# Kernel tuning notes

Hardware: AMD Instinct MI355X
Metric: run time of the kernel (lower is better)

Reference implementation:

```python
import jax, jax.numpy as jnp
import numpy as np

C = 256
CQK = C // 8  # 32

def setup_inputs() -> dict:
    key = jax.random.key(0)
    ks = jax.random.split(key, 8)
    N, L = 8, 4096
    x = jax.random.normal(ks[0], (N, C, L), dtype=jnp.float32)
    s = 1.0 / np.sqrt(C)
    Wq = jax.random.normal(ks[1], (CQK, C), dtype=jnp.float32) * s
    bq = jnp.zeros((CQK,), dtype=jnp.float32)
    Wk = jax.random.normal(ks[2], (CQK, C), dtype=jnp.float32) * s
    bk = jnp.zeros((CQK,), dtype=jnp.float32)
    Wv = jax.random.normal(ks[3], (C, C), dtype=jnp.float32) * s
    bv = jnp.zeros((C,), dtype=jnp.float32)
    gamma = jnp.ones((1,), dtype=jnp.float32) * 0.5  # nonzero so output depends on attention
    return {"x": x, "Wq": Wq, "bq": bq, "Wk": Wk, "bk": bk, "Wv": Wv, "bv": bv, "gamma": gamma}

def reference(x, Wq, bq, Wk, bk, Wv, bv, gamma):
    # conv1d with kernel_size=1 == pointwise linear over channel dim
    q = jnp.einsum('ncl,oc->nol', x, Wq) + bq[None, :, None]   # (N, C/8, L)
    k = jnp.einsum('ncl,oc->nol', x, Wk) + bk[None, :, None]   # (N, C/8, L)
    v = jnp.einsum('ncl,oc->nol', x, Wv) + bv[None, :, None]   # (N, C, L)
    # energy[n, i, j] = q[n, :, i] . k[n, :, j]
    energy = jnp.einsum('nci,ncj->nij', q, k)                  # (N, L, L)
    attention = jax.nn.softmax(energy, axis=-1)
    # out[n, c, i] = sum_j v[n, c, j] * attention[n, i, j]
    out = jnp.einsum('ncj,nij->nci', v, attention)             # (N, C, L)
    return gamma * out + x
```

## Files before the change

kernel.cpp:

```cpp
#include <hip/hip_runtime.h>
#include <hip/hip_bf16.h>

#define NB 8
#define CC 256
#define LL 4096
#define CQ 32

typedef __bf16 bf16x8 __attribute__((ext_vector_type(8)));
typedef float f32x4 __attribute__((ext_vector_type(4)));
typedef unsigned short u16x4 __attribute__((ext_vector_type(4)));

union B8u { bf16x8 b; u16x4 h[2]; };
union P4u { u16x4 u; __bf16 e[4]; };

#define WS_QT  ((size_t)0)
#define WS_KT  ((size_t)1048576)
#define WS_VV  ((size_t)2097152)
#define WS_WQ  ((size_t)18874368)
#define WS_BQ  ((size_t)18882560)
#define WS_WK  ((size_t)18882592)
#define WS_BK  ((size_t)18890784)
#define WS_WV  ((size_t)18890816)
#define WS_BV  ((size_t)18956352)

__device__ __forceinline__ bool tag_is_bf16(const void* gamma_raw) {
  return *(const unsigned short*)gamma_raw != 0;
}
__device__ __forceinline__ float cvt_load(const void* p, size_t i, bool b16) {
  return b16 ? (float)((const __bf16*)p)[i] : ((const float*)p)[i];
}

__global__ __launch_bounds__(256) void convert_wb_kernel(
    const void* __restrict__ Wq, const void* __restrict__ bq,
    const void* __restrict__ Wk, const void* __restrict__ bk,
    const void* __restrict__ Wv, const void* __restrict__ bv,
    const void* __restrict__ gm, __bf16* __restrict__ ws)
{
  const bool b16 = tag_is_bf16(gm);
  int t = blockIdx.x * 256 + threadIdx.x;
  for (int i = t; i < 82240; i += 32 * 256) {
    float v; size_t dof;
    if (i < 8192)       { v = cvt_load(Wq, i, b16);         dof = WS_WQ + i; }
    else if (i < 8224)  { v = cvt_load(bq, i - 8192, b16);  dof = WS_BQ + (i - 8192); }
    else if (i < 16416) { v = cvt_load(Wk, i - 8224, b16);  dof = WS_WK + (i - 8224); }
    else if (i < 16448) { v = cvt_load(bk, i - 16416, b16); dof = WS_BK + (i - 16416); }
    else if (i < 81984) { v = cvt_load(Wv, i - 16448, b16); dof = WS_WV + (i - 16448); }
    else                { v = cvt_load(bv, i - 81984, b16); dof = WS_BV + (i - 81984); }
    ws[dof] = (__bf16)v;
  }
}

__global__ __launch_bounds__(256, 2) void proj_kernel(
    const void* __restrict__ x_raw, const void* __restrict__ gm_raw,
    __bf16* __restrict__ ws)
{
  const bool b16 = tag_is_bf16(gm_raw);
  const int bid = blockIdx.x;
  const int n = bid & 7, l0 = (bid >> 3) * 64;
  const int tid = threadIdx.x;
  const int w = tid >> 6, lane = tid & 63, li = lane & 15, qd = lane >> 4;

  __shared__ __align__(16) __bf16 tmp[64][72];
  __shared__ __align__(16) __bf16 xlt[64][264];

  for (int cb = 0; cb < 4; ++cb) {
    __syncthreads();
    #pragma unroll
    for (int p = 0; p < 2; ++p) {
      int cc = (tid >> 3) + p * 32;
      int lc = (tid & 7) * 8;
      size_t off = (size_t)n * CC * LL + (size_t)(cb * 64 + cc) * LL + l0 + lc;
      bf16x8 val;
      if (b16) {
        val = *(const bf16x8*)((const __bf16*)x_raw + off);
      } else {
        const float* xf = (const float*)x_raw + off;
        f32x4 a = *(const f32x4*)xf;
        f32x4 b = *(const f32x4*)(xf + 4);
        #pragma unroll
        for (int s = 0; s < 4; ++s) { val[s] = (__bf16)a[s]; val[s + 4] = (__bf16)b[s]; }
      }
      *(bf16x8*)(&tmp[cc][lc]) = val;
    }
    __syncthreads();
    #pragma unroll
    for (int p = 0; p < 2; ++p) {
      int lx = (tid >> 3) + p * 32;
      int cw = (tid & 7) * 8;
      bf16x8 o;
      #pragma unroll
      for (int s = 0; s < 8; ++s) o[s] = tmp[cw + s][lx];
      *(bf16x8*)(&xlt[lx][cb * 64 + cw]) = o;
    }
  }
  __syncthreads();

  const __bf16* Wqk = (w < 2) ? (ws + WS_WQ) : (ws + WS_WK);
  const __bf16* Wv  = ws + WS_WV;
  const int obase = (w & 1) * 16;

  f32x4 vacc[4][4];
  f32x4 qkacc[4];
  #pragma unroll
  for (int a = 0; a < 4; ++a) {
    qkacc[a] = f32x4{0, 0, 0, 0};
    #pragma unroll
    for (int b = 0; b < 4; ++b) vacc[a][b] = f32x4{0, 0, 0, 0};
  }

  for (int k0 = 0; k0 < CC; k0 += 32) {
    bf16x8 xf[4];
    #pragma unroll
    for (int lt = 0; lt < 4; ++lt)
      xf[lt] = *(const bf16x8*)(&xlt[lt * 16 + li][k0 + qd * 8]);
    bf16x8 wa = *(const bf16x8*)(Wqk + (size_t)(obase + li) * CC + k0 + qd * 8);
    #pragma unroll
    for (int lt = 0; lt < 4; ++lt)
      qkacc[lt] = __builtin_amdgcn_mfma_f32_16x16x32_bf16(wa, xf[lt], qkacc[lt], 0, 0, 0);
    #pragma unroll
    for (int ct = 0; ct < 4; ++ct) {
      bf16x8 wb = *(const bf16x8*)(Wv + (size_t)(w * 64 + ct * 16 + li) * CC + k0 + qd * 8);
      #pragma unroll
      for (int lt = 0; lt < 4; ++lt)
        vacc[lt][ct] = __builtin_amdgcn_mfma_f32_16x16x32_bf16(xf[lt], wb, vacc[lt][ct], 0, 0, 0);
    }
  }

  {
    const __bf16* bqk = (w < 2) ? (ws + WS_BQ) : (ws + WS_BK);
    __bf16* dqk = ((w < 2) ? (ws + WS_QT) : (ws + WS_KT)) + (size_t)n * LL * CQ;
    float bf[4];
    #pragma unroll
    for (int rr = 0; rr < 4; ++rr) bf[rr] = (float)bqk[obase + qd * 4 + rr];
    #pragma unroll
    for (int lt = 0; lt < 4; ++lt) {
      P4u pk;
      #pragma unroll
      for (int rr = 0; rr < 4; ++rr) pk.e[rr] = (__bf16)(qkacc[lt][rr] + bf[rr]);
      *(u16x4*)(dqk + (size_t)(l0 + lt * 16 + li) * CQ + obase + qd * 4) = pk.u;
    }
  }
  {
    __bf16* dv = ws + WS_VV + (size_t)n * 128 * CC * 32;
    #pragma unroll
    for (int ct = 0; ct < 4; ++ct) {
      int c = w * 64 + ct * 16 + li;
      float bvf = (float)(ws + WS_BV)[c];
      #pragma unroll
      for (int lt = 0; lt < 4; ++lt) {
        int jl = lt * 16 + qd * 4;
        int jb = (l0 + jl) >> 5, jj = jl & 31;
        P4u pk;
        #pragma unroll
        for (int rr = 0; rr < 4; ++rr) pk.e[rr] = (__bf16)(vacc[lt][ct][rr] + bvf);
        *(u16x4*)(dv + ((size_t)jb * CC + c) * 32 + jj) = pk.u;
      }
    }
  }
}

__global__ __launch_bounds__(1024, 4) void attn_kernel(
    const __bf16* __restrict__ ws, const void* __restrict__ x_raw,
    const void* __restrict__ gamma_raw, void* __restrict__ out_raw)
{
  const int bid = blockIdx.x;
  const int n = bid & 7, iblk = (bid >> 3) * 128;
  const int tid = threadIdx.x, w = tid >> 6, lane = tid & 63;
  const int li = lane & 15, qd = lane >> 4;
  const int it = w & 7, jh = w >> 3;
  const int cg = w & 7, jg = w >> 3;

  const __bf16* qtn = ws + WS_QT + (size_t)n * LL * CQ;
  const __bf16* ktn = ws + WS_KT + (size_t)n * LL * CQ;
  const __bf16* v2n = ws + WS_VV + (size_t)n * 128 * CC * 32;

  __shared__ __align__(16) __bf16 plds[2][4][8][16][36];
  __shared__ __align__(16) float  lbuf[16][16];
  __shared__ __align__(16) __bf16 olds[256][72];
  float* scratch = (float*)&plds[0][0][0][0][0];

  bf16x8 qfrag = *(const bf16x8*)(qtn + (size_t)(iblk + it * 16 + li) * CQ + qd * 8);
  const f32x4 zero = {0.f, 0.f, 0.f, 0.f};

  f32x4 oacc[16];
  #pragma unroll
  for (int t = 0; t < 16; ++t) oacc[t] = zero;
  float lp = 0.f;

  bf16x8 kf[4];
  #pragma unroll
  for (int u = 0; u < 4; ++u)
    kf[u] = *(const bf16x8*)(ktn + (size_t)(jh * 64 + u * 16 + li) * CQ + qd * 8);

  for (int js = 0; js < LL; js += 128) {
    const int buf = (js >> 7) & 1;
    bf16x8 vf[4];
    #pragma unroll
    for (int s = 0; s < 2; ++s) {
      const int jb = (js >> 5) + jg * 2 + s;
      #pragma unroll
      for (int ct = 0; ct < 2; ++ct)
        vf[s * 2 + ct] = *(const bf16x8*)(v2n + ((size_t)jb * CC + cg * 32 + ct * 16 + li) * 32 + qd * 8);
    }
    #pragma unroll
    for (int u = 0; u < 4; ++u) {
      f32x4 s = __builtin_amdgcn_mfma_f32_16x16x32_bf16(kf[u], qfrag, zero, 0, 0, 0);
      P4u pk;
      #pragma unroll
      for (int r = 0; r < 4; ++r) {
        float e = __expf(s[r]); lp += e; pk.e[r] = (__bf16)e;
      }
      *(u16x4*)(&plds[buf][jh * 2 + (u >> 1)][it][li][(u & 1) * 16 + qd * 4]) = pk.u;
    }
    {
      const int jn = (js + 128 < LL) ? (js + 128) : 0;
      #pragma unroll
      for (int u = 0; u < 4; ++u)
        kf[u] = *(const bf16x8*)(ktn + (size_t)(jn + jh * 64 + u * 16 + li) * CQ + qd * 8);
    }
    __syncthreads();
    #pragma unroll
    for (int s = 0; s < 2; ++s) {
      #pragma unroll
      for (int tt = 0; tt < 8; ++tt) {
        B8u ap;
        ap.b = *(const bf16x8*)(&plds[buf][jg * 2 + s][tt][li][qd * 8]);
        oacc[tt * 2 + 0] = __builtin_amdgcn_mfma_f32_16x16x32_bf16(ap.b, vf[s * 2 + 0], oacc[tt * 2 + 0], 0, 0, 0);
        oacc[tt * 2 + 1] = __builtin_amdgcn_mfma_f32_16x16x32_bf16(ap.b, vf[s * 2 + 1], oacc[tt * 2 + 1], 0, 0, 0);
      }
    }
  }

  lp += __shfl_xor(lp, 16);
  lp += __shfl_xor(lp, 32);
  lbuf[it * 2 + jh][li] = lp;
  __syncthreads();

  #pragma unroll
  for (int r = 0; r < 2; ++r) {
    if (jg == 1 && (cg >> 2) == r) {
      float* d = scratch + (size_t)(cg & 3) * 4096;
      #pragma unroll
      for (int t = 0; t < 16; ++t)
        *(f32x4*)(d + t * 256 + lane * 4) = oacc[t];
    }
    __syncthreads();
    if (jg == 0 && (cg >> 2) == r) {
      const float* s = scratch + (size_t)(cg & 3) * 4096;
      #pragma unroll
      for (int t = 0; t < 16; ++t)
        oacc[t] += *(const f32x4*)(s + t * 256 + lane * 4);
    }
    __syncthreads();
  }

  const bool b16 = tag_is_bf16(gamma_raw);
  const float gma = b16 ? (float)(*(const __bf16*)gamma_raw)
                        : (*(const float*)gamma_raw);

  f32x4 gi[8];
  if (jg == 0) {
    #pragma unroll
    for (int pp = 0; pp < 8; ++pp) {
      f32x4 l0v = *(const f32x4*)(&lbuf[pp * 2 + 0][qd * 4]);
      f32x4 l1v = *(const f32x4*)(&lbuf[pp * 2 + 1][qd * 4]);
      #pragma unroll
      for (int rr = 0; rr < 4; ++rr) gi[pp][rr] = gma / (l0v[rr] + l1v[rr]);
    }
  }

  const int ec = tid >> 5, i2 = (tid & 31) * 2;
  #pragma unroll
  for (int h = 0; h < 2; ++h) {
    if (jg == 0) {
      #pragma unroll
      for (int pi = 0; pi < 4; ++pi) {
        const int pp = h * 4 + pi;
        #pragma unroll
        for (int ct = 0; ct < 2; ++ct) {
          P4u pk;
          #pragma unroll
          for (int rr = 0; rr < 4; ++rr)
            pk.e[rr] = (__bf16)(oacc[pp * 2 + ct][rr] * gi[pp][rr]);
          *(u16x4*)(&olds[cg * 32 + ct * 16 + li][pi * 16 + qd * 4]) = pk.u;
        }
      }
    }
    __syncthreads();
    const int ibase = iblk + h * 64;
    if (b16) {
      const __bf16* xn = (const __bf16*)x_raw + (size_t)n * CC * LL;
      __bf16* outn = (__bf16*)out_raw + (size_t)n * CC * LL;
      for (int c = ec; c < CC; c += 32) {
        unsigned int ov = *(const unsigned int*)(&olds[c][i2]);
        unsigned int xv = *(const unsigned int*)(xn + (size_t)c * LL + ibase + i2);
        const __bf16* op = (const __bf16*)&ov;
        const __bf16* xp = (const __bf16*)&xv;
        unsigned int res;
        __bf16* rp = (__bf16*)&res;
        rp[0] = (__bf16)((float)op[0] + (float)xp[0]);
        rp[1] = (__bf16)((float)op[1] + (float)xp[1]);
        *(unsigned int*)(outn + (size_t)c * LL + ibase + i2) = res;
      }
    } else {
      const float* xn = (const float*)x_raw + (size_t)n * CC * LL;
      float* outn = (float*)out_raw + (size_t)n * CC * LL;
      for (int c = ec; c < CC; c += 32) {
        unsigned int ov = *(const unsigned int*)(&olds[c][i2]);
        const __bf16* op = (const __bf16*)&ov;
        float2 xv = *(const float2*)(xn + (size_t)c * LL + ibase + i2);
        float2 res;
        res.x = (float)op[0] + xv.x;
        res.y = (float)op[1] + xv.y;
        *(float2*)(outn + (size_t)c * LL + ibase + i2) = res;
      }
    }
    __syncthreads();
  }
}

extern "C" void kernel_launch(void* const* d_in, const int* in_sizes, int n_in,
                              void* d_out, int out_size, void* d_ws, size_t ws_size,
                              hipStream_t stream) {
  (void)in_sizes; (void)n_in; (void)out_size; (void)ws_size;
  __bf16* ws = (__bf16*)d_ws;

  hipLaunchKernelGGL(convert_wb_kernel, dim3(32), dim3(256), 0, stream,
                     d_in[1], d_in[2], d_in[3], d_in[4], d_in[5], d_in[6],
                     d_in[7], ws);
  hipLaunchKernelGGL(proj_kernel, dim3(512), dim3(256), 0, stream,
                     d_in[0], d_in[7], ws);
  hipLaunchKernelGGL(attn_kernel, dim3(256), dim3(1024), 0, stream,
                     (const __bf16*)ws, d_in[0], d_in[7], d_out);
}
```

Measured before the change: 200.5 us.

## Switch attention kernel to 32x32x16 MFMA tiles with swizzled LDS and exp2

Rewrites the attention kernel's inner loop to use 32x32x16 bf16 MFMA instructions instead of 16x16x32, changing the wave-to-tile mapping, the P-tile LDS layout (now a flat 128x128 buffer with XOR swizzle), and the cross-wave reduction. Q is pre-scaled by log2(e) in the projection kernel so the softmax can use the raw exp2 instruction instead of __expf. The normalizer is computed once into a shared linv array. Launch bounds drop from 4 to 2 blocks per CU hint, trading occupancy for more registers and larger accumulator tiles.

```diff
diff --git a/kernel.cpp b/kernel.cpp
--- a/kernel.cpp
+++ b/kernel.cpp
@@ -8,9 +8,9 @@
 
 typedef __bf16 bf16x8 __attribute__((ext_vector_type(8)));
 typedef float f32x4 __attribute__((ext_vector_type(4)));
+typedef float f32x16 __attribute__((ext_vector_type(16)));
 typedef unsigned short u16x4 __attribute__((ext_vector_type(4)));
 
-union B8u { bf16x8 b; u16x4 h[2]; };
 union P4u { u16x4 u; __bf16 e[4]; };
 
 #define WS_QT  ((size_t)0)
@@ -128,6 +128,7 @@
 
   {
     const __bf16* bqk = (w < 2) ? (ws + WS_BQ) : (ws + WS_BK);
+    const float qscl = (w < 2) ? 1.4426950408889634f : 1.0f;
     __bf16* dqk = ((w < 2) ? (ws + WS_QT) : (ws + WS_KT)) + (size_t)n * LL * CQ;
     float bf[4];
     #pragma unroll
@@ -136,7 +137,7 @@
     for (int lt = 0; lt < 4; ++lt) {
       P4u pk;
       #pragma unroll
-      for (int rr = 0; rr < 4; ++rr) pk.e[rr] = (__bf16)(qkacc[lt][rr] + bf[rr]);
+      for (int rr = 0; rr < 4; ++rr) pk.e[rr] = (__bf16)((qkacc[lt][rr] + bf[rr]) * qscl);
       *(u16x4*)(dqk + (size_t)(l0 + lt * 16 + li) * CQ + obase + qd * 4) = pk.u;
     }
   }
@@ -159,97 +160,131 @@
   }
 }
 
-__global__ __launch_bounds__(1024, 4) void attn_kernel(
+__global__ __launch_bounds__(1024, 2) void attn_kernel(
     const __bf16* __restrict__ ws, const void* __restrict__ x_raw,
     const void* __restrict__ gamma_raw, void* __restrict__ out_raw)
 {
   const int bid = blockIdx.x;
   const int n = bid & 7, iblk = (bid >> 3) * 128;
   const int tid = threadIdx.x, w = tid >> 6, lane = tid & 63;
-  const int li = lane & 15, qd = lane >> 4;
-  const int it = w & 7, jh = w >> 3;
-  const int cg = w & 7, jg = w >> 3;
+  const int cl = lane & 31, hi = lane >> 5;
+  const int jt = w & 3, it2 = w >> 2;
+  const int ig = w & 1, cg = (w >> 1) & 3, jg = w >> 3;
 
   const __bf16* qtn = ws + WS_QT + (size_t)n * LL * CQ;
   const __bf16* ktn = ws + WS_KT + (size_t)n * LL * CQ;
   const __bf16* v2n = ws + WS_VV + (size_t)n * 128 * CC * 32;
 
-  __shared__ __align__(16) __bf16 plds[2][4][8][16][36];
-  __shared__ __align__(16) float  lbuf[16][16];
-  __shared__ __align__(16) __bf16 olds[256][72];
-  float* scratch = (float*)&plds[0][0][0][0][0];
-
-  bf16x8 qfrag = *(const bf16x8*)(qtn + (size_t)(iblk + it * 16 + li) * CQ + qd * 8);
-  const f32x4 zero = {0.f, 0.f, 0.f, 0.f};
-
-  f32x4 oacc[16];
-  #pragma unroll
-  for (int t = 0; t < 16; ++t) oacc[t] = zero;
+  __shared__ __align__(16) __bf16 plds[2][128][128];
+  __shared__ __align__(16) float  lbuf[4][128];
+  __shared__ __align__(16) float  linv[128];
+  __shared__ __align__(16) __bf16 olds[256][68];
+  float* scratch = (float*)&plds[0][0][0];
+  char* pbase = (char*)&plds[0][0][0];
+
+  const unsigned swzp = (unsigned)(cl & 15) << 4;
+
+  const unsigned pw_base = (unsigned)(it2 * 32 + cl) * 256;
+  unsigned wcol[4];
+  #pragma unroll
+  for (int g = 0; g < 4; ++g)
+    wcol[g] = (unsigned)((jt * 64 + 16 * g + 8 * hi) ^ (int)swzp);
+
+  const unsigned rrow0 = (unsigned)((ig * 2 + 0) * 32 + cl) * 256;
+  const unsigned rrow1 = (unsigned)((ig * 2 + 1) * 32 + cl) * 256;
+  unsigned rcol[4];
+  #pragma unroll
+  for (int ch = 0; ch < 4; ++ch)
+    rcol[ch] = (unsigned)((jg * 128 + ch * 32 + hi * 16) ^ (int)swzp);
+
+  const bf16x8 qf0 = *(const bf16x8*)(qtn + (size_t)(iblk + it2 * 32 + cl) * CQ + hi * 8);
+  const bf16x8 qf1 = *(const bf16x8*)(qtn + (size_t)(iblk + it2 * 32 + cl) * CQ + 16 + hi * 8);
+
+  const f32x16 z16 = {0.f,0.f,0.f,0.f, 0.f,0.f,0.f,0.f,
+                      0.f,0.f,0.f,0.f, 0.f,0.f,0.f,0.f};
+  f32x16 acc[2][2];
+  acc[0][0] = z16; acc[0][1] = z16; acc[1][0] = z16; acc[1][1] = z16;
   float lp = 0.f;
 
-  bf16x8 kf[4];
-  #pragma unroll
-  for (int u = 0; u < 4; ++u)
-    kf[u] = *(const bf16x8*)(ktn + (size_t)(jh * 64 + u * 16 + li) * CQ + qd * 8);
+  bf16x8 kf0 = *(const bf16x8*)(ktn + (size_t)(jt * 32 + cl) * CQ + hi * 8);
+  bf16x8 kf1 = *(const bf16x8*)(ktn + (size_t)(jt * 32 + cl) * CQ + 16 + hi * 8);
 
   for (int js = 0; js < LL; js += 128) {
-    const int buf = (js >> 7) & 1;
-    bf16x8 vf[4];
-    #pragma unroll
-    for (int s = 0; s < 2; ++s) {
-      const int jb = (js >> 5) + jg * 2 + s;
+    char* pbyte = pbase + (((js >> 7) & 1) << 15);
+    bf16x8 vf[4][2];
+    #pragma unroll
+    for (int ch = 0; ch < 4; ++ch) {
+      const int jb = (js >> 5) + jg * 2 + (ch >> 1);
+      const int jlo = (ch & 1) * 16 + hi * 8;
       #pragma unroll
       for (int ct = 0; ct < 2; ++ct)
-        vf[s * 2 + ct] = *(const bf16x8*)(v2n + ((size_t)jb * CC + cg * 32 + ct * 16 + li) * 32 + qd * 8);
-    }
-    #pragma unroll
-    for (int u = 0; u < 4; ++u) {
-      f32x4 s = __builtin_amdgcn_mfma_f32_16x16x32_bf16(kf[u], qfrag, zero, 0, 0, 0);
+        vf[ch][ct] = *(const bf16x8*)(v2n + ((size_t)jb * CC + cg * 64 + ct * 32 + cl) * 32 + jlo);
+    }
+    const int jn = (js + 128 < LL) ? (js + 128) : 0;
+    const bf16x8 kn0 = *(const bf16x8*)(ktn + (size_t)(jn + jt * 32 + cl) * CQ + hi * 8);
+    const bf16x8 kn1 = *(const bf16x8*)(ktn + (size_t)(jn + jt * 32 + cl) * CQ + 16 + hi * 8);
+
+    f32x16 sv = __builtin_amdgcn_mfma_f32_32x32x16_bf16(kf0, qf0, z16, 0, 0, 0);
+    sv = __builtin_amdgcn_mfma_f32_32x32x16_bf16(kf1, qf1, sv, 0, 0, 0);
+    #pragma unroll
+    for (int g = 0; g < 4; ++g) {
+      float e0 = __builtin_amdgcn_exp2f(sv[g * 4 + 0]);
+      float e1 = __builtin_amdgcn_exp2f(sv[g * 4 + 1]);
+      float e2 = __builtin_amdgcn_exp2f(sv[g * 4 + 2]);
+      float e3 = __builtin_amdgcn_exp2f(sv[g * 4 + 3]);
+      lp += (e0 + e1) + (e2 + e3);
       P4u pk;
-      #pragma unroll
-      for (int r = 0; r < 4; ++r) {
-        float e = __expf(s[r]); lp += e; pk.e[r] = (__bf16)e;
-      }
-      *(u16x4*)(&plds[buf][jh * 2 + (u >> 1)][it][li][(u & 1) * 16 + qd * 4]) = pk.u;
-    }
-    {
-      const int jn = (js + 128 < LL) ? (js + 128) : 0;
-      #pragma unroll
-      for (int u = 0; u < 4; ++u)
-        kf[u] = *(const bf16x8*)(ktn + (size_t)(jn + jh * 64 + u * 16 + li) * CQ + qd * 8);
-    }
-    __syncthreads();
-    #pragma unroll
-    for (int s = 0; s < 2; ++s) {
-      #pragma unroll
-      for (int tt = 0; tt < 8; ++tt) {
-        B8u ap;
-        ap.b = *(const bf16x8*)(&plds[buf][jg * 2 + s][tt][li][qd * 8]);
-        oacc[tt * 2 + 0] = __builtin_amdgcn_mfma_f32_16x16x32_bf16(ap.b, vf[s * 2 + 0], oacc[tt * 2 + 0], 0, 0, 0);
-        oacc[tt * 2 + 1] = __builtin_amdgcn_mfma_f32_16x16x32_bf16(ap.b, vf[s * 2 + 1], oacc[tt * 2 + 1], 0, 0, 0);
-      }
-    }
-  }
-
-  lp += __shfl_xor(lp, 16);
+      pk.e[0] = (__bf16)e0; pk.e[1] = (__bf16)e1;
+      pk.e[2] = (__bf16)e2; pk.e[3] = (__bf16)e3;
+      *(u16x4*)(pbyte + pw_base + wcol[g]) = pk.u;
+    }
+    kf0 = kn0; kf1 = kn1;
+    __syncthreads();
+    #pragma unroll
+    for (int ch = 0; ch < 4; ++ch) {
+      const bf16x8 ap0 = *(const bf16x8*)(pbyte + rrow0 + rcol[ch]);
+      const bf16x8 ap1 = *(const bf16x8*)(pbyte + rrow1 + rcol[ch]);
+      acc[0][0] = __builtin_amdgcn_mfma_f32_32x32x16_bf16(ap0, vf[ch][0], acc[0][0], 0, 0, 0);
+      acc[0][1] = __builtin_amdgcn_mfma_f32_32x32x16_bf16(ap0, vf[ch][1], acc[0][1], 0, 0, 0);
+      acc[1][0] = __builtin_amdgcn_mfma_f32_32x32x16_bf16(ap1, vf[ch][0], acc[1][0], 0, 0, 0);
+      acc[1][1] = __builtin_amdgcn_mfma_f32_32x32x16_bf16(ap1, vf[ch][1], acc[1][1], 0, 0, 0);
+    }
+  }
+
   lp += __shfl_xor(lp, 32);
-  lbuf[it * 2 + jh][li] = lp;
+  if (hi == 0) lbuf[jt][it2 * 32 + cl] = lp;
   __syncthreads();
 
   #pragma unroll
   for (int r = 0; r < 2; ++r) {
-    if (jg == 1 && (cg >> 2) == r) {
-      float* d = scratch + (size_t)(cg & 3) * 4096;
-      #pragma unroll
-      for (int t = 0; t < 16; ++t)
-        *(f32x4*)(d + t * 256 + lane * 4) = oacc[t];
-    }
-    __syncthreads();
-    if (jg == 0 && (cg >> 2) == r) {
-      const float* s = scratch + (size_t)(cg & 3) * 4096;
-      #pragma unroll
-      for (int t = 0; t < 16; ++t)
-        oacc[t] += *(const f32x4*)(s + t * 256 + lane * 4);
+    if (jg == 1 && (cg & 1) == r) {
+      float* d = scratch + (size_t)(ig * 2 + (cg >> 1)) * 4096 + lane * 4;
+      #pragma unroll
+      for (int tl = 0; tl < 2; ++tl)
+        #pragma unroll
+        for (int ct = 0; ct < 2; ++ct)
+          #pragma unroll
+          for (int q = 0; q < 4; ++q) {
+            f32x4 v4 = { acc[tl][ct][q * 4 + 0], acc[tl][ct][q * 4 + 1],
+                         acc[tl][ct][q * 4 + 2], acc[tl][ct][q * 4 + 3] };
+            *(f32x4*)(d + (tl * 8 + ct * 4 + q) * 256) = v4;
+          }
+    }
+    __syncthreads();
+    if (jg == 0 && (cg & 1) == r) {
+      const float* s0 = scratch + (size_t)(ig * 2 + (cg >> 1)) * 4096 + lane * 4;
+      #pragma unroll
+      for (int tl = 0; tl < 2; ++tl)
+        #pragma unroll
+        for (int ct = 0; ct < 2; ++ct)
+          #pragma unroll
+          for (int q = 0; q < 4; ++q) {
+            const f32x4 v4 = *(const f32x4*)(s0 + (tl * 8 + ct * 4 + q) * 256);
+            acc[tl][ct][q * 4 + 0] += v4[0];
+            acc[tl][ct][q * 4 + 1] += v4[1];
+            acc[tl][ct][q * 4 + 2] += v4[2];
+            acc[tl][ct][q * 4 + 3] += v4[3];
+          }
     }
     __syncthreads();
   }
@@ -257,32 +292,29 @@
   const bool b16 = tag_is_bf16(gamma_raw);
   const float gma = b16 ? (float)(*(const __bf16*)gamma_raw)
                         : (*(const float*)gamma_raw);
-
-  f32x4 gi[8];
-  if (jg == 0) {
-    #pragma unroll
-    for (int pp = 0; pp < 8; ++pp) {
-      f32x4 l0v = *(const f32x4*)(&lbuf[pp * 2 + 0][qd * 4]);
-      f32x4 l1v = *(const f32x4*)(&lbuf[pp * 2 + 1][qd * 4]);
-      #pragma unroll
-      for (int rr = 0; rr < 4; ++rr) gi[pp][rr] = gma / (l0v[rr] + l1v[rr]);
-    }
-  }
+  if (tid < 128)
+    linv[tid] = gma / (lbuf[0][tid] + lbuf[1][tid] + lbuf[2][tid] + lbuf[3][tid]);
+  __syncthreads();
 
   const int ec = tid >> 5, i2 = (tid & 31) * 2;
   #pragma unroll
   for (int h = 0; h < 2; ++h) {
-    if (jg == 0) {
-      #pragma unroll
-      for (int pi = 0; pi < 4; ++pi) {
-        const int pp = h * 4 + pi;
+    if (jg == 0 && ig == h) {
+      #pragma unroll
+      for (int tl = 0; tl < 2; ++tl) {
         #pragma unroll
         for (int ct = 0; ct < 2; ++ct) {
-          P4u pk;
+          const int c = cg * 64 + ct * 32 + cl;
           #pragma unroll
-          for (int rr = 0; rr < 4; ++rr)
-            pk.e[rr] = (__bf16)(oacc[pp * 2 + ct][rr] * gi[pp][rr]);
-          *(u16x4*)(&olds[cg * 32 + ct * 16 + li][pi * 16 + qd * 4]) = pk.u;
+          for (int g = 0; g < 4; ++g) {
+            const int io = tl * 32 + 8 * g + 4 * hi;
+            const f32x4 gv = *(const f32x4*)&linv[h * 64 + io];
+            P4u pk;
+            #pragma unroll
+            for (int rr = 0; rr < 4; ++rr)
+              pk.e[rr] = (__bf16)(acc[tl][ct][g * 4 + rr] * gv[rr]);
+            *(u16x4*)(&olds[c][io]) = pk.u;
+          }
         }
       }
     }
```

New measurement: 370.4 us. 1.85x slower.

## Halve attention block size and drop split-j cross-wave accumulator reduction

Applied to the files above, without the earlier changes.

Each attention block now covers 64 query rows with 512 threads instead of 128 rows with 1024 threads, and the grid doubles to 512 blocks. Each wave now owns a 32-channel slice across the full 128-key step, so the split-key partial accumulators and their shared-memory reduction with extra barriers go away. V fragments are reloaded mid-step for the second key half, with a sched_barrier between the halves. This cuts accumulator registers and epilogue synchronisation and gives more blocks for load balance. In exchange, each block does twice the V loads per query row and K is re-read by twice as many blocks.

```diff
diff --git a/kernel.cpp b/kernel.cpp
--- a/kernel.cpp
+++ b/kernel.cpp
@@ -159,32 +159,31 @@
   }
 }
 
-__global__ __launch_bounds__(1024, 4) void attn_kernel(
+__global__ __launch_bounds__(512, 4) void attn_kernel(
     const __bf16* __restrict__ ws, const void* __restrict__ x_raw,
     const void* __restrict__ gamma_raw, void* __restrict__ out_raw)
 {
   const int bid = blockIdx.x;
-  const int n = bid & 7, iblk = (bid >> 3) * 128;
+  const int n = bid & 7, iblk = (bid >> 3) * 64;
   const int tid = threadIdx.x, w = tid >> 6, lane = tid & 63;
   const int li = lane & 15, qd = lane >> 4;
-  const int it = w & 7, jh = w >> 3;
-  const int cg = w & 7, jg = w >> 3;
+  const int it = w & 3, jh = w >> 2;
+  const int cg = w;
 
   const __bf16* qtn = ws + WS_QT + (size_t)n * LL * CQ;
   const __bf16* ktn = ws + WS_KT + (size_t)n * LL * CQ;
   const __bf16* v2n = ws + WS_VV + (size_t)n * 128 * CC * 32;
 
-  __shared__ __align__(16) __bf16 plds[2][4][8][16][36];
-  __shared__ __align__(16) float  lbuf[16][16];
+  __shared__ __align__(16) __bf16 plds[2][4][4][16][36];
+  __shared__ __align__(16) float  lbuf[8][16];
   __shared__ __align__(16) __bf16 olds[256][72];
-  float* scratch = (float*)&plds[0][0][0][0][0];
 
   bf16x8 qfrag = *(const bf16x8*)(qtn + (size_t)(iblk + it * 16 + li) * CQ + qd * 8);
   const f32x4 zero = {0.f, 0.f, 0.f, 0.f};
 
-  f32x4 oacc[16];
-  #pragma unroll
-  for (int t = 0; t < 16; ++t) oacc[t] = zero;
+  f32x4 oacc[8];
+  #pragma unroll
+  for (int t = 0; t < 8; ++t) oacc[t] = zero;
   float lp = 0.f;
 
   bf16x8 kf[4];
@@ -197,7 +196,7 @@
     bf16x8 vf[4];
     #pragma unroll
     for (int s = 0; s < 2; ++s) {
-      const int jb = (js >> 5) + jg * 2 + s;
+      const int jb = (js >> 5) + s;
       #pragma unroll
       for (int ct = 0; ct < 2; ++ct)
         vf[s * 2 + ct] = *(const bf16x8*)(v2n + ((size_t)jb * CC + cg * 32 + ct * 16 + li) * 32 + qd * 8);
@@ -222,9 +221,27 @@
     #pragma unroll
     for (int s = 0; s < 2; ++s) {
       #pragma unroll
-      for (int tt = 0; tt < 8; ++tt) {
+      for (int tt = 0; tt < 4; ++tt) {
         B8u ap;
-        ap.b = *(const bf16x8*)(&plds[buf][jg * 2 + s][tt][li][qd * 8]);
+        ap.b = *(const bf16x8*)(&plds[buf][s][tt][li][qd * 8]);
+        oacc[tt * 2 + 0] = __builtin_amdgcn_mfma_f32_16x16x32_bf16(ap.b, vf[s * 2 + 0], oacc[tt * 2 + 0], 0, 0, 0);
+        oacc[tt * 2 + 1] = __builtin_amdgcn_mfma_f32_16x16x32_bf16(ap.b, vf[s * 2 + 1], oacc[tt * 2 + 1], 0, 0, 0);
+      }
+    }
+    __builtin_amdgcn_sched_barrier(0);
+    #pragma unroll
+    for (int s = 0; s < 2; ++s) {
+      const int jb = (js >> 5) + 2 + s;
+      #pragma unroll
+      for (int ct = 0; ct < 2; ++ct)
+        vf[s * 2 + ct] = *(const bf16x8*)(v2n + ((size_t)jb * CC + cg * 32 + ct * 16 + li) * 32 + qd * 8);
+    }
+    #pragma unroll
+    for (int s = 0; s < 2; ++s) {
+      #pragma unroll
+      for (int tt = 0; tt < 4; ++tt) {
+        B8u ap;
+        ap.b = *(const bf16x8*)(&plds[buf][2 + s][tt][li][qd * 8]);
         oacc[tt * 2 + 0] = __builtin_amdgcn_mfma_f32_16x16x32_bf16(ap.b, vf[s * 2 + 0], oacc[tt * 2 + 0], 0, 0, 0);
         oacc[tt * 2 + 1] = __builtin_amdgcn_mfma_f32_16x16x32_bf16(ap.b, vf[s * 2 + 1], oacc[tt * 2 + 1], 0, 0, 0);
       }
@@ -236,86 +253,60 @@
   lbuf[it * 2 + jh][li] = lp;
   __syncthreads();
 
-  #pragma unroll
-  for (int r = 0; r < 2; ++r) {
-    if (jg == 1 && (cg >> 2) == r) {
-      float* d = scratch + (size_t)(cg & 3) * 4096;
-      #pragma unroll
-      for (int t = 0; t < 16; ++t)
-        *(f32x4*)(d + t * 256 + lane * 4) = oacc[t];
-    }
-    __syncthreads();
-    if (jg == 0 && (cg >> 2) == r) {
-      const float* s = scratch + (size_t)(cg & 3) * 4096;
-      #pragma unroll
-      for (int t = 0; t < 16; ++t)
-        oacc[t] += *(const f32x4*)(s + t * 256 + lane * 4);
-    }
-    __syncthreads();
-  }
-
   const bool b16 = tag_is_bf16(gamma_raw);
   const float gma = b16 ? (float)(*(const __bf16*)gamma_raw)
                         : (*(const float*)gamma_raw);
 
-  f32x4 gi[8];
-  if (jg == 0) {
-    #pragma unroll
-    for (int pp = 0; pp < 8; ++pp) {
-      f32x4 l0v = *(const f32x4*)(&lbuf[pp * 2 + 0][qd * 4]);
-      f32x4 l1v = *(const f32x4*)(&lbuf[pp * 2 + 1][qd * 4]);
-      #pragma unroll
-      for (int rr = 0; rr < 4; ++rr) gi[pp][rr] = gma / (l0v[rr] + l1v[rr]);
-    }
-  }
+  f32x4 gi[4];
+  #pragma unroll
+  for (int tt = 0; tt < 4; ++tt) {
+    f32x4 l0v = *(const f32x4*)(&lbuf[tt * 2 + 0][qd * 4]);
+    f32x4 l1v = *(const f32x4*)(&lbuf[tt * 2 + 1][qd * 4]);
+    #pragma unroll
+    for (int rr = 0; rr < 4; ++rr) gi[tt][rr] = gma / (l0v[rr] + l1v[rr]);
+  }
+
+  #pragma unroll
+  for (int tt = 0; tt < 4; ++tt) {
+    #pragma unroll
+    for (int ct = 0; ct < 2; ++ct) {
+      P4u pk;
+      #pragma unroll
+      for (int rr = 0; rr < 4; ++rr)
+        pk.e[rr] = (__bf16)(oacc[tt * 2 + ct][rr] * gi[tt][rr]);
+      *(u16x4*)(&olds[cg * 32 + ct * 16 + li][tt * 16 + qd * 4]) = pk.u;
+    }
+  }
+  __syncthreads();
 
   const int ec = tid >> 5, i2 = (tid & 31) * 2;
-  #pragma unroll
-  for (int h = 0; h < 2; ++h) {
-    if (jg == 0) {
-      #pragma unroll
-      for (int pi = 0; pi < 4; ++pi) {
-        const int pp = h * 4 + pi;
-        #pragma unroll
-        for (int ct = 0; ct < 2; ++ct) {
-          P4u pk;
-          #pragma unroll
-          for (int rr = 0; rr < 4; ++rr)
-            pk.e[rr] = (__bf16)(oacc[pp * 2 + ct][rr] * gi[pp][rr]);
-          *(u16x4*)(&olds[cg * 32 + ct * 16 + li][pi * 16 + qd * 4]) = pk.u;
-        }
-      }
-    }
-    __syncthreads();
-    const int ibase = iblk + h * 64;
-    if (b16) {
-      const __bf16* xn = (const __bf16*)x_raw + (size_t)n * CC * LL;
-      __bf16* outn = (__bf16*)out_raw + (size_t)n * CC * LL;
-      for (int c = ec; c < CC; c += 32) {
-        unsigned int ov = *(const unsigned int*)(&olds[c][i2]);
-        unsigned int xv = *(const unsigned int*)(xn + (size_t)c * LL + ibase + i2);
-        const __bf16* op = (const __bf16*)&ov;
-        const __bf16* xp = (const __bf16*)&xv;
-        unsigned int res;
-        __bf16* rp = (__bf16*)&res;
-        rp[0] = (__bf16)((float)op[0] + (float)xp[0]);
-        rp[1] = (__bf16)((float)op[1] + (float)xp[1]);
-        *(unsigned int*)(outn + (size_t)c * LL + ibase + i2) = res;
-      }
-    } else {
-      const float* xn = (const float*)x_raw + (size_t)n * CC * LL;
-      float* outn = (float*)out_raw + (size_t)n * CC * LL;
-      for (int c = ec; c < CC; c += 32) {
-        unsigned int ov = *(const unsigned int*)(&olds[c][i2]);
-        const __bf16* op = (const __bf16*)&ov;
-        float2 xv = *(const float2*)(xn + (size_t)c * LL + ibase + i2);
-        float2 res;
-        res.x = (float)op[0] + xv.x;
-        res.y = (float)op[1] + xv.y;
-        *(float2*)(outn + (size_t)c * LL + ibase + i2) = res;
-      }
-    }
-    __syncthreads();
+  const int ibase = iblk;
+  if (b16) {
+    const __bf16* xn = (const __bf16*)x_raw + (size_t)n * CC * LL;
+    __bf16* outn = (__bf16*)out_raw + (size_t)n * CC * LL;
+    for (int c = ec; c < CC; c += 16) {
+      unsigned int ov = *(const unsigned int*)(&olds[c][i2]);
+      unsigned int xv = *(const unsigned int*)(xn + (size_t)c * LL + ibase + i2);
+      const __bf16* op = (const __bf16*)&ov;
+      const __bf16* xp = (const __bf16*)&xv;
+      unsigned int res;
+      __bf16* rp = (__bf16*)&res;
+      rp[0] = (__bf16)((float)op[0] + (float)xp[0]);
+      rp[1] = (__bf16)((float)op[1] + (float)xp[1]);
+      *(unsigned int*)(outn + (size_t)c * LL + ibase + i2) = res;
+    }
+  } else {
+    const float* xn = (const float*)x_raw + (size_t)n * CC * LL;
+    float* outn = (float*)out_raw + (size_t)n * CC * LL;
+    for (int c = ec; c < CC; c += 16) {
+      unsigned int ov = *(const unsigned int*)(&olds[c][i2]);
+      const __bf16* op = (const __bf16*)&ov;
+      float2 xv = *(const float2*)(xn + (size_t)c * LL + ibase + i2);
+      float2 res;
+      res.x = (float)op[0] + xv.x;
+      res.y = (float)op[1] + xv.y;
+      *(float2*)(outn + (size_t)c * LL + ibase + i2) = res;
+    }
   }
 }
 
@@ -330,6 +321,6 @@
                      d_in[7], ws);
   hipLaunchKernelGGL(proj_kernel, dim3(512), dim3(256), 0, stream,
                      d_in[0], d_in[7], ws);
-  hipLaunchKernelGGL(attn_kernel, dim3(256), dim3(1024), 0, stream,
+  hipLaunchKernelGGL(attn_kernel, dim3(512), dim3(512), 0, stream,
                      (const __bf16*)ws, d_in[0], d_in[7], d_out);
 }
```

Measured after the change: 215.0 us. 1.07x slower.

## Warp-specialize attention into softmax producers and PV consumers with double-buffered P

Applied to the files above, without the earlier changes.

Splits the 16 waves into 8 producer waves that compute QK^T, exponentiate and write P tiles to a double-buffered LDS region, and 8 consumer waves that run the P·V MFMAs one tile behind. This drops the cross-wave reduction of split-j partial outputs and lets the exp and QK work overlap with the PV matrix multiplies. It also permutes the V workspace layout so the P fragment ordering matches, and widens the output staging buffer to hold all 128 rows at once. The risk is imbalance between producer and consumer work, plus heavier register pressure in the consumer waves with 16 accumulators.

```diff
diff --git a/kernel.cpp b/kernel.cpp
--- a/kernel.cpp
+++ b/kernel.cpp
@@ -10,7 +10,6 @@
 typedef float f32x4 __attribute__((ext_vector_type(4)));
 typedef unsigned short u16x4 __attribute__((ext_vector_type(4)));
 
-union B8u { bf16x8 b; u16x4 h[2]; };
 union P4u { u16x4 u; __bf16 e[4]; };
 
 #define WS_QT  ((size_t)0)
@@ -149,11 +148,12 @@
       #pragma unroll
       for (int lt = 0; lt < 4; ++lt) {
         int jl = lt * 16 + qd * 4;
-        int jb = (l0 + jl) >> 5, jj = jl & 31;
+        int jb = (l0 + jl) >> 5;
+        int pos = qd * 8 + (lt & 1) * 4;
         P4u pk;
         #pragma unroll
         for (int rr = 0; rr < 4; ++rr) pk.e[rr] = (__bf16)(vacc[lt][ct][rr] + bvf);
-        *(u16x4*)(dv + ((size_t)jb * CC + c) * 32 + jj) = pk.u;
+        *(u16x4*)(dv + ((size_t)jb * CC + c) * 32 + pos) = pk.u;
       }
     }
   }
@@ -167,132 +167,144 @@
   const int n = bid & 7, iblk = (bid >> 3) * 128;
   const int tid = threadIdx.x, w = tid >> 6, lane = tid & 63;
   const int li = lane & 15, qd = lane >> 4;
-  const int it = w & 7, jh = w >> 3;
-  const int cg = w & 7, jg = w >> 3;
 
   const __bf16* qtn = ws + WS_QT + (size_t)n * LL * CQ;
   const __bf16* ktn = ws + WS_KT + (size_t)n * LL * CQ;
   const __bf16* v2n = ws + WS_VV + (size_t)n * 128 * CC * 32;
 
-  __shared__ __align__(16) __bf16 plds[2][4][8][16][36];
-  __shared__ __align__(16) float  lbuf[16][16];
-  __shared__ __align__(16) __bf16 olds[256][72];
-  float* scratch = (float*)&plds[0][0][0][0][0];
-
-  bf16x8 qfrag = *(const bf16x8*)(qtn + (size_t)(iblk + it * 16 + li) * CQ + qd * 8);
-  const f32x4 zero = {0.f, 0.f, 0.f, 0.f};
-
-  f32x4 oacc[16];
-  #pragma unroll
-  for (int t = 0; t < 16; ++t) oacc[t] = zero;
-  float lp = 0.f;
-
-  bf16x8 kf[4];
-  #pragma unroll
-  for (int u = 0; u < 4; ++u)
-    kf[u] = *(const bf16x8*)(ktn + (size_t)(jh * 64 + u * 16 + li) * CQ + qd * 8);
-
-  for (int js = 0; js < LL; js += 128) {
-    const int buf = (js >> 7) & 1;
-    bf16x8 vf[4];
-    #pragma unroll
-    for (int s = 0; s < 2; ++s) {
-      const int jb = (js >> 5) + jg * 2 + s;
-      #pragma unroll
-      for (int ct = 0; ct < 2; ++ct)
-        vf[s * 2 + ct] = *(const bf16x8*)(v2n + ((size_t)jb * CC + cg * 32 + ct * 16 + li) * 32 + qd * 8);
-    }
-    #pragma unroll
-    for (int u = 0; u < 4; ++u) {
-      f32x4 s = __builtin_amdgcn_mfma_f32_16x16x32_bf16(kf[u], qfrag, zero, 0, 0, 0);
-      P4u pk;
-      #pragma unroll
-      for (int r = 0; r < 4; ++r) {
-        float e = __expf(s[r]); lp += e; pk.e[r] = (__bf16)e;
-      }
-      *(u16x4*)(&plds[buf][jh * 2 + (u >> 1)][it][li][(u & 1) * 16 + qd * 4]) = pk.u;
-    }
-    {
-      const int jn = (js + 128 < LL) ? (js + 128) : 0;
-      #pragma unroll
-      for (int u = 0; u < 4; ++u)
-        kf[u] = *(const bf16x8*)(ktn + (size_t)(jn + jh * 64 + u * 16 + li) * CQ + qd * 8);
-    }
-    __syncthreads();
-    #pragma unroll
-    for (int s = 0; s < 2; ++s) {
-      #pragma unroll
-      for (int tt = 0; tt < 8; ++tt) {
-        B8u ap;
-        ap.b = *(const bf16x8*)(&plds[buf][jg * 2 + s][tt][li][qd * 8]);
-        oacc[tt * 2 + 0] = __builtin_amdgcn_mfma_f32_16x16x32_bf16(ap.b, vf[s * 2 + 0], oacc[tt * 2 + 0], 0, 0, 0);
-        oacc[tt * 2 + 1] = __builtin_amdgcn_mfma_f32_16x16x32_bf16(ap.b, vf[s * 2 + 1], oacc[tt * 2 + 1], 0, 0, 0);
-      }
-    }
-  }
-
-  lp += __shfl_xor(lp, 16);
-  lp += __shfl_xor(lp, 32);
-  lbuf[it * 2 + jh][li] = lp;
-  __syncthreads();
-
-  #pragma unroll
-  for (int r = 0; r < 2; ++r) {
-    if (jg == 1 && (cg >> 2) == r) {
-      float* d = scratch + (size_t)(cg & 3) * 4096;
-      #pragma unroll
-      for (int t = 0; t < 16; ++t)
-        *(f32x4*)(d + t * 256 + lane * 4) = oacc[t];
-    }
-    __syncthreads();
-    if (jg == 0 && (cg >> 2) == r) {
-      const float* s = scratch + (size_t)(cg & 3) * 4096;
-      #pragma unroll
-      for (int t = 0; t < 16; ++t)
-        oacc[t] += *(const f32x4*)(s + t * 256 + lane * 4);
-    }
-    __syncthreads();
-  }
+  __shared__ __align__(16) __bf16 plds[2][4][128][40];
+  __shared__ __align__(16) float  lbuf[4][128];
+  __shared__ __align__(16) __bf16 olds[256][132];
+  char* pbase = (char*)&plds[0][0][0][0];
 
   const bool b16 = tag_is_bf16(gamma_raw);
   const float gma = b16 ? (float)(*(const __bf16*)gamma_raw)
                         : (*(const float*)gamma_raw);
-
-  f32x4 gi[8];
-  if (jg == 0) {
-    #pragma unroll
-    for (int pp = 0; pp < 8; ++pp) {
-      f32x4 l0v = *(const f32x4*)(&lbuf[pp * 2 + 0][qd * 4]);
-      f32x4 l1v = *(const f32x4*)(&lbuf[pp * 2 + 1][qd * 4]);
-      #pragma unroll
-      for (int rr = 0; rr < 4; ++rr) gi[pp][rr] = gma / (l0v[rr] + l1v[rr]);
-    }
+  const f32x4 zero = {0.f, 0.f, 0.f, 0.f};
+
+  if (w < 8) {
+    const int it = w & 1, jh = w >> 1;
+    const unsigned pw = (unsigned)jh * 10240 + (unsigned)(it * 64 + li) * 80
+                      + (unsigned)qd * 16;
+
+    bf16x8 qf[4];
+    #pragma unroll
+    for (int ii = 0; ii < 4; ++ii)
+      qf[ii] = *(const bf16x8*)(qtn + (size_t)(iblk + it * 64 + ii * 16 + li) * CQ + qd * 8);
+
+    bf16x8 kf0 = *(const bf16x8*)(ktn + (size_t)(jh * 32 + li) * CQ + qd * 8);
+    bf16x8 kf1 = *(const bf16x8*)(ktn + (size_t)(jh * 32 + 16 + li) * CQ + qd * 8);
+
+    float lp[4] = {0.f, 0.f, 0.f, 0.f};
+    float lq[4] = {0.f, 0.f, 0.f, 0.f};
+
+    #define PRODUCE(t)                                                         \
+    {                                                                          \
+      char* pbyte = pbase + (((t) >> 7) & 1) * 40960;                          \
+      _Pragma("unroll")                                                        \
+      for (int ii = 0; ii < 4; ++ii) {                                         \
+        f32x4 s0 = __builtin_amdgcn_mfma_f32_16x16x32_bf16(kf0, qf[ii], zero, 0, 0, 0); \
+        f32x4 s1 = __builtin_amdgcn_mfma_f32_16x16x32_bf16(kf1, qf[ii], zero, 0, 0, 0); \
+        bf16x8 p8;                                                             \
+        _Pragma("unroll")                                                      \
+        for (int r = 0; r < 4; ++r) {                                          \
+          float e0 = __expf(s0[r]); lp[ii] += e0; p8[r] = (__bf16)e0;          \
+          float e1 = __expf(s1[r]); lq[ii] += e1; p8[4 + r] = (__bf16)e1;      \
+        }                                                                      \
+        *(bf16x8*)(pbyte + pw + ii * 1280) = p8;                               \
+      }                                                                        \
+      const int tn = ((t) + 128 < LL) ? (t) + 128 : 0;                         \
+      kf0 = *(const bf16x8*)(ktn + (size_t)(tn + jh * 32 + li) * CQ + qd * 8); \
+      kf1 = *(const bf16x8*)(ktn + (size_t)(tn + jh * 32 + 16 + li) * CQ + qd * 8); \
+    }
+
+    PRODUCE(0);
+    __syncthreads();
+    for (int js = 0; js < LL; js += 128) {
+      const int t = js + 128;
+      if (t < LL) PRODUCE(t);
+      __syncthreads();
+    }
+    #undef PRODUCE
+
+    #pragma unroll
+    for (int ii = 0; ii < 4; ++ii) {
+      float v = lp[ii] + lq[ii];
+      v += __shfl_xor(v, 16);
+      v += __shfl_xor(v, 32);
+      if (qd == 0) lbuf[jh][it * 64 + ii * 16 + li] = v;
+    }
+    __syncthreads();
+    __syncthreads();
+  } else {
+    const int cw = w - 8;
+    const int ch = cw & 3, ih = cw >> 2;
+    const unsigned pr = (unsigned)(ih * 64 + li) * 80 + (unsigned)qd * 16;
+
+    f32x4 oacc[4][4];
+    #pragma unroll
+    for (int a = 0; a < 4; ++a)
+      #pragma unroll
+      for (int b = 0; b < 4; ++b) oacc[a][b] = zero;
+
+    __syncthreads();
+    for (int js = 0; js < LL; js += 128) {
+      const char* pb = pbase + ((js >> 7) & 1) * 40960;
+      #pragma unroll
+      for (int q = 0; q < 4; ++q) {
+        const int jb = (js >> 5) + q;
+        bf16x8 vf[4];
+        #pragma unroll
+        for (int ct = 0; ct < 4; ++ct)
+          vf[ct] = *(const bf16x8*)(v2n + ((size_t)jb * CC + ch * 64 + ct * 16 + li) * 32 + qd * 8);
+        #pragma unroll
+        for (int it = 0; it < 4; ++it) {
+          const bf16x8 ap = *(const bf16x8*)(pb + q * 10240 + pr + it * 1280);
+          oacc[it][0] = __builtin_amdgcn_mfma_f32_16x16x32_bf16(ap, vf[0], oacc[it][0], 0, 0, 0);
+          oacc[it][1] = __builtin_amdgcn_mfma_f32_16x16x32_bf16(ap, vf[1], oacc[it][1], 0, 0, 0);
+          oacc[it][2] = __builtin_amdgcn_mfma_f32_16x16x32_bf16(ap, vf[2], oacc[it][2], 0, 0, 0);
+          oacc[it][3] = __builtin_amdgcn_mfma_f32_16x16x32_bf16(ap, vf[3], oacc[it][3], 0, 0, 0);
+        }
+      }
+      __syncthreads();
+    }
+
+    __syncthreads();
+    #pragma unroll
+    for (int it = 0; it < 4; ++it) {
+      const int ib = ih * 64 + it * 16 + qd * 4;
+      f32x4 s = *(const f32x4*)&lbuf[0][ib];
+      {
+        const f32x4 s1 = *(const f32x4*)&lbuf[1][ib];
+        const f32x4 s2 = *(const f32x4*)&lbuf[2][ib];
+        const f32x4 s3 = *(const f32x4*)&lbuf[3][ib];
+        #pragma unroll
+        for (int rr = 0; rr < 4; ++rr) s[rr] = s[rr] + s1[rr] + s2[rr] + s3[rr];
+      }
+      f32x4 gi;
+      #pragma unroll
+      for (int rr = 0; rr < 4; ++rr) gi[rr] = gma / s[rr];
+      #pragma unroll
+      for (int ct = 0; ct < 4; ++ct) {
+        P4u pk;
+        #pragma unroll
+        for (int rr = 0; rr < 4; ++rr)
+          pk.e[rr] = (__bf16)(oacc[it][ct][rr] * gi[rr]);
+        *(u16x4*)(&olds[ch * 64 + ct * 16 + li][ib]) = pk.u;
+      }
+    }
+    __syncthreads();
   }
 
   const int ec = tid >> 5, i2 = (tid & 31) * 2;
   #pragma unroll
   for (int h = 0; h < 2; ++h) {
-    if (jg == 0) {
-      #pragma unroll
-      for (int pi = 0; pi < 4; ++pi) {
-        const int pp = h * 4 + pi;
-        #pragma unroll
-        for (int ct = 0; ct < 2; ++ct) {
-          P4u pk;
-          #pragma unroll
-          for (int rr = 0; rr < 4; ++rr)
-            pk.e[rr] = (__bf16)(oacc[pp * 2 + ct][rr] * gi[pp][rr]);
-          *(u16x4*)(&olds[cg * 32 + ct * 16 + li][pi * 16 + qd * 4]) = pk.u;
-        }
-      }
-    }
-    __syncthreads();
     const int ibase = iblk + h * 64;
     if (b16) {
       const __bf16* xn = (const __bf16*)x_raw + (size_t)n * CC * LL;
       __bf16* outn = (__bf16*)out_raw + (size_t)n * CC * LL;
       for (int c = ec; c < CC; c += 32) {
-        unsigned int ov = *(const unsigned int*)(&olds[c][i2]);
+        unsigned int ov = *(const unsigned int*)(&olds[c][h * 64 + i2]);
         unsigned int xv = *(const unsigned int*)(xn + (size_t)c * LL + ibase + i2);
         const __bf16* op = (const __bf16*)&ov;
         const __bf16* xp = (const __bf16*)&xv;
@@ -306,7 +318,7 @@
       const float* xn = (const float*)x_raw + (size_t)n * CC * LL;
       float* outn = (float*)out_raw + (size_t)n * CC * LL;
       for (int c = ec; c < CC; c += 32) {
-        unsigned int ov = *(const unsigned int*)(&olds[c][i2]);
+        unsigned int ov = *(const unsigned int*)(&olds[c][h * 64 + i2]);
         const __bf16* op = (const __bf16*)&ov;
         float2 xv = *(const float2*)(xn + (size_t)c * LL + ibase + i2);
         float2 res;
@@ -315,7 +327,6 @@
         *(float2*)(outn + (size_t)c * LL + ibase + i2) = res;
       }
     }
-    __syncthreads();
   }
 }
 
```

Measured after the change: 204.7 us. +2.1%, slower.
